# Optimization experiments

Hardware: AMD Instinct MI355X
Metric: run time of the kernel (lower is better)

Reference implementation:

```python
import jax, jax.numpy as jnp
import numpy as np

N, E, D, L, V = 200000, 500000, 128, 5, 8
BN_EPS = 1e-5


def _bn(h, g, b, m, v):
    # eval-mode BatchNorm1d with running stats
    return (h - m) * jax.lax.rsqrt(v + BN_EPS) * g + b


def setup_inputs() -> dict:
    key = jax.random.key(0)
    ks = iter(jax.random.split(key, 40))
    nk = lambda: next(ks)
    f = lambda shape: jax.random.normal(nk(), shape, jnp.float32) * 0.05
    inp = {}
    inp["x"] = jax.random.normal(nk(), (N, 12), jnp.float32)
    inp["edge_index"] = jax.random.randint(nk(), (2, E), 0, N, dtype=jnp.int32)
    inp["edge_attr"] = jax.random.randint(nk(), (E, 3), 0, V, dtype=jnp.int32)
    # atom encoder: Lin(12,D) -> BN -> ReLU -> Lin(D,D) -> BN -> ReLU -> Lin(D,D)
    inp["ae_W1"] = f((12, D)); inp["ae_b1"] = jnp.zeros((D,), jnp.float32)
    inp["ae_g1"] = jnp.ones((D,), jnp.float32); inp["ae_be1"] = jnp.zeros((D,), jnp.float32)
    inp["ae_m1"] = f((D,)); inp["ae_v1"] = jax.random.uniform(nk(), (D,), jnp.float32) + 0.5
    inp["ae_W2"] = f((D, D)); inp["ae_b2"] = jnp.zeros((D,), jnp.float32)
    inp["ae_g2"] = jnp.ones((D,), jnp.float32); inp["ae_be2"] = jnp.zeros((D,), jnp.float32)
    inp["ae_m2"] = f((D,)); inp["ae_v2"] = jax.random.uniform(nk(), (D,), jnp.float32) + 0.5
    inp["ae_W3"] = f((D, D)); inp["ae_b3"] = jnp.zeros((D,), jnp.float32)
    # per-layer GIN params (stacked over L)
    inp["bond_emb"] = f((L, 3, V, D))
    inp["eps"] = jnp.zeros((L,), jnp.float32)
    inp["mlp_W1"] = f((L, D, D)); inp["mlp_b1"] = jnp.zeros((L, D), jnp.float32)
    inp["mlp_g"] = jnp.ones((L, D), jnp.float32); inp["mlp_be"] = jnp.zeros((L, D), jnp.float32)
    inp["mlp_m"] = f((L, D)); inp["mlp_v"] = jax.random.uniform(nk(), (L, D), jnp.float32) + 0.5
    inp["mlp_W2"] = f((L, D, D)); inp["mlp_b2"] = jnp.zeros((L, D), jnp.float32)
    # per-layer outer BatchNorm
    inp["out_g"] = jnp.ones((L, D), jnp.float32); inp["out_be"] = jnp.zeros((L, D), jnp.float32)
    inp["out_m"] = f((L, D)); inp["out_v"] = jax.random.uniform(nk(), (L, D), jnp.float32) + 0.5
    return inp


def reference(x, edge_index, edge_attr,
              ae_W1, ae_b1, ae_g1, ae_be1, ae_m1, ae_v1,
              ae_W2, ae_b2, ae_g2, ae_be2, ae_m2, ae_v2,
              ae_W3, ae_b3,
              bond_emb, eps, mlp_W1, mlp_b1, mlp_g, mlp_be, mlp_m, mlp_v,
              mlp_W2, mlp_b2, out_g, out_be, out_m, out_v):
    n_nodes = x.shape[0]
    src, dst = edge_index[0], edge_index[1]
    # atom encoder
    h = jax.nn.relu(_bn(x @ ae_W1 + ae_b1, ae_g1, ae_be1, ae_m1, ae_v1))
    h = jax.nn.relu(_bn(h @ ae_W2 + ae_b2, ae_g2, ae_be2, ae_m2, ae_v2))
    h = h @ ae_W3 + ae_b3  # [N, D]
    n_layers = bond_emb.shape[0]
    for l in range(n_layers):
        # BondEncoder: sum of per-feature embeddings -> [E, D]
        be = bond_emb[l]
        e_emb = be[0][edge_attr[:, 0]] + be[1][edge_attr[:, 1]] + be[2][edge_attr[:, 2]]
        # message: relu(x_j + edge_emb); aggregate: scatter-add at dst
        msg = jax.nn.relu(h[src] + e_emb)
        agg = jax.ops.segment_sum(msg, dst, num_segments=n_nodes)
        z = (1.0 + eps[l]) * h + agg
        # GIN MLP: Lin -> BN -> ReLU -> Lin
        z = jax.nn.relu(_bn(z @ mlp_W1[l] + mlp_b1[l], mlp_g[l], mlp_be[l], mlp_m[l], mlp_v[l]))
        z = z @ mlp_W2[l] + mlp_b2[l]
        # outer BatchNorm; ReLU on all but last layer (dropout is identity in eval)
        z = _bn(z, out_g[l], out_be[l], out_m[l], out_v[l])
        if l < n_layers - 1:
            z = jax.nn.relu(z)
        h = z
    return h  # JK='last'
```

## Files before the change

kernel.cpp:

```cpp
#include <hip/hip_runtime.h>
#include <hip/hip_bf16.h>
#include <cstdint>
#include <cstddef>

#define D 128
#define NNODES 200000
#define NEDGES 500000
#define NLAYERS 5
#define BN_EPS 1e-5f
#define MAXDEG 24

typedef __attribute__((ext_vector_type(8))) short bf16x8;
typedef __attribute__((ext_vector_type(4))) float f32x4;

__device__ __forceinline__ unsigned short f2bf(float f) {
    union { float f; unsigned int u; } x; x.f = f;
    unsigned int r = (x.u + 0x7FFFu + ((x.u >> 16) & 1u)) >> 16;
    return (unsigned short)r;
}
__device__ __forceinline__ float bf2f(unsigned short u) {
    union { unsigned int u; float f; } x; x.u = ((unsigned int)u) << 16; return x.f;
}

__global__ void k_zero(int* __restrict__ p, int n) {
    int i = blockIdx.x * 256 + threadIdx.x;
    if (i < n) p[i] = 0;
}

__global__ void k_fill_edges(const int* __restrict__ ei, const int* __restrict__ ea,
                             int* __restrict__ deg, int* __restrict__ elist, int n_edges) {
    int e = blockIdx.x * 256 + threadIdx.x;
    if (e >= n_edges) return;
    int dst = ei[n_edges + e];
    int src = ei[e];
    int a0 = ea[e * 3], a1 = ea[e * 3 + 1], a2 = ea[e * 3 + 2];
    int rec = src | (a0 << 18) | (a1 << 21) | (a2 << 24);
    int pos = atomicAdd(&deg[dst], 1);
    if (pos < MAXDEG) elist[dst * MAXDEG + pos] = rec;
}

__global__ void k_prep_w(const float* __restrict__ aeW2, const float* __restrict__ aeW3,
                         const float* __restrict__ mlpW1, const float* __restrict__ mlpW2,
                         unsigned short* __restrict__ wbt) {
    int m = blockIdx.x >> 3;
    int s = (blockIdx.x & 7) * 256 + threadIdx.x;
    int f = s >> 4;
    int kc = (s & 15) * 8;
    const float* W;
    if (m == 0) W = aeW2;
    else if (m == 1) W = aeW3;
    else if (m < 7) W = mlpW1 + (size_t)(m - 2) * D * D;
    else W = mlpW2 + (size_t)(m - 7) * D * D;
    unsigned short tmp[8];
#pragma unroll
    for (int j = 0; j < 8; ++j) tmp[j] = f2bf(W[(size_t)(kc + j) * D + f]);
    *(int4*)(wbt + (size_t)m * D * D + (size_t)f * D + kc) = *(int4*)tmp;
}

__global__ void k_bondsum(const float* __restrict__ bond, unsigned short* __restrict__ bsum) {
    int idx = blockIdx.x;
    int l = idx >> 9, combo = idx & 511;
    int a0 = combo & 7, a1 = (combo >> 3) & 7, a2 = (combo >> 6) & 7;
    int f = threadIdx.x;
    const float* bl = bond + (size_t)l * 3 * 8 * 128;
    bsum[(size_t)idx * 128 + f] =
        f2bf(bl[a0 * 128 + f] + bl[1024 + a1 * 128 + f] + bl[2048 + a2 * 128 + f]);
}

__global__ void k_ae1(const float* __restrict__ x, const float* __restrict__ W,
                      const float* __restrict__ b, const float* __restrict__ g,
                      const float* __restrict__ be, const float* __restrict__ m,
                      const float* __restrict__ v, unsigned short* __restrict__ out) {
    __shared__ float sW[12][128];
    int tid = threadIdx.x;
    for (int i = tid; i < 12 * 128; i += 256) sW[i >> 7][i & 127] = W[i];
    int f0 = (tid & 31) * 4;
    int g8 = tid >> 5;
    float4 bb = *(const float4*)(b + f0);
    float4 gg = *(const float4*)(g + f0);
    float4 ee = *(const float4*)(be + f0);
    float4 mm = *(const float4*)(m + f0);
    float4 vv = *(const float4*)(v + f0);
    float A0 = gg.x * rsqrtf(vv.x + BN_EPS), S0 = (bb.x - mm.x) * A0 + ee.x;
    float A1 = gg.y * rsqrtf(vv.y + BN_EPS), S1 = (bb.y - mm.y) * A1 + ee.y;
    float A2 = gg.z * rsqrtf(vv.z + BN_EPS), S2 = (bb.z - mm.z) * A2 + ee.z;
    float A3 = gg.w * rsqrtf(vv.w + BN_EPS), S3 = (bb.w - mm.w) * A3 + ee.w;
    __syncthreads();
    for (int n = blockIdx.x * 8 + g8; n < NNODES; n += gridDim.x * 8) {
        const float4* xr = (const float4*)(x + (size_t)n * 12);
        float4 x0 = xr[0], x1 = xr[1], x2 = xr[2];
        float xv[12] = {x0.x, x0.y, x0.z, x0.w, x1.x, x1.y, x1.z, x1.w,
                        x2.x, x2.y, x2.z, x2.w};
        float a0 = 0.f, a1 = 0.f, a2 = 0.f, a3 = 0.f;
#pragma unroll
        for (int k = 0; k < 12; ++k) {
            float4 wv = *(float4*)&sW[k][f0];
            a0 += xv[k] * wv.x; a1 += xv[k] * wv.y;
            a2 += xv[k] * wv.z; a3 += xv[k] * wv.w;
        }
        unsigned short o[4];
        o[0] = f2bf(fmaxf(a0 * A0 + S0, 0.f));
        o[1] = f2bf(fmaxf(a1 * A1 + S1, 0.f));
        o[2] = f2bf(fmaxf(a2 * A2 + S2, 0.f));
        o[3] = f2bf(fmaxf(a3 * A3 + S3, 0.f));
        *(uint2*)(out + (size_t)n * D + f0) = *(uint2*)o;
    }
}

__launch_bounds__(256, 8)
__global__ void k_agg(const unsigned short* __restrict__ hin,
                      const unsigned short* __restrict__ bsum,
                      const float* __restrict__ eps_arr, int layer,
                      const int* __restrict__ deg, const int* __restrict__ elist,
                      unsigned short* __restrict__ out) {
    int tid = threadIdx.x;
    int f4 = tid & 31;
    int n = blockIdx.x * 8 + (tid >> 5);
    int dgr = min(deg[n], MAXDEG);
    int rec = (f4 < MAXDEG) ? elist[(size_t)n * MAXDEG + f4] : 0;
    float epsv = 1.f + eps_arr[layer];
    ushort4 hs = *(const ushort4*)(hin + (size_t)n * D + f4 * 4);
    float z0 = epsv * bf2f(hs.x), z1 = epsv * bf2f(hs.y);
    float z2 = epsv * bf2f(hs.z), z3 = epsv * bf2f(hs.w);

    ushort4 hv[6]; ushort4 bv[6]; int rr[6];
#pragma unroll
    for (int j = 0; j < 6; ++j) {
        rr[j] = __shfl(rec, j, 32);
        if (j < dgr) {
            hv[j] = *(const ushort4*)(hin + (size_t)(rr[j] & 0x3FFFF) * D + f4 * 4);
            bv[j] = *(const ushort4*)(bsum + (size_t)((rr[j] >> 18) & 511) * D + f4 * 4);
        }
    }
#pragma unroll
    for (int j = 0; j < 6; ++j) {
        if (j < dgr) {
            z0 += fmaxf(bf2f(hv[j].x) + bf2f(bv[j].x), 0.f);
            z1 += fmaxf(bf2f(hv[j].y) + bf2f(bv[j].y), 0.f);
            z2 += fmaxf(bf2f(hv[j].z) + bf2f(bv[j].z), 0.f);
            z3 += fmaxf(bf2f(hv[j].w) + bf2f(bv[j].w), 0.f);
        }
    }
    for (int base = 6; base < dgr; base += 4) {
        ushort4 hw[4]; ushort4 bw[4]; int rt[4];
#pragma unroll
        for (int j = 0; j < 4; ++j) {
            rt[j] = __shfl(rec, base + j, 32);
            if (base + j < dgr) {
                hw[j] = *(const ushort4*)(hin + (size_t)(rt[j] & 0x3FFFF) * D + f4 * 4);
                bw[j] = *(const ushort4*)(bsum + (size_t)((rt[j] >> 18) & 511) * D + f4 * 4);
            }
        }
#pragma unroll
        for (int j = 0; j < 4; ++j) {
            if (base + j < dgr) {
                z0 += fmaxf(bf2f(hw[j].x) + bf2f(bw[j].x), 0.f);
                z1 += fmaxf(bf2f(hw[j].y) + bf2f(bw[j].y), 0.f);
                z2 += fmaxf(bf2f(hw[j].z) + bf2f(bw[j].z), 0.f);
                z3 += fmaxf(bf2f(hw[j].w) + bf2f(bw[j].w), 0.f);
            }
        }
    }
    unsigned short o[4] = {f2bf(z0), f2bf(z1), f2bf(z2), f2bf(z3)};
    *(uint2*)(out + (size_t)n * D + f4 * 4) = *(uint2*)o;
}

#define SWZ(row, bytecol) (((row) * 256 + (bytecol)) ^ (((row) & 7) << 4))
template<int OUTF32>
__launch_bounds__(512, 6)
__global__ void k_mlp2(const unsigned short* __restrict__ hin,
                       const unsigned short* __restrict__ W1t,
                       const float* __restrict__ b1,
                       const float* __restrict__ g1, const float* __restrict__ be1,
                       const float* __restrict__ m1, const float* __restrict__ v1,
                       const unsigned short* __restrict__ W2t,
                       const float* __restrict__ b2,
                       const float* __restrict__ g2, const float* __restrict__ be2,
                       const float* __restrict__ m2, const float* __restrict__ v2,
                       unsigned short* __restrict__ outb, float* __restrict__ outf,
                       int do_bn2, int do_relu2) {
    __shared__ char sA[16384];
    __shared__ char sZ[16384];
    int tid = threadIdx.x;
    size_t nb = (size_t)blockIdx.x * 64;
    int lane = tid & 63;
    int w = tid >> 6;
    int arow = lane & 15;
    int kq = (lane >> 4) * 8;
    int c = w * 16 + arow;

    bf16x8 w1f[4], w2f[4];
#pragma unroll
    for (int kb = 0; kb < 4; ++kb) {
        w1f[kb] = *(const bf16x8*)(W1t + (size_t)c * D + kb * 32 + kq);
        w2f[kb] = *(const bf16x8*)(W2t + (size_t)c * D + kb * 32 + kq);
    }
#pragma unroll
    for (int i = 0; i < 2; ++i) {
        int s = tid + i * 512;
        int r = s >> 4, cc = (s & 15) * 16;
        *(int4*)(sA + SWZ(r, cc)) = *(const int4*)((const char*)hin + (nb + r) * 256 + cc);
    }
    __syncthreads();

    f32x4 acc[4];
#pragma unroll
    for (int rt = 0; rt < 4; ++rt) acc[rt] = (f32x4){0.f, 0.f, 0.f, 0.f};
#pragma unroll
    for (int kb = 0; kb < 4; ++kb) {
        int k0 = kb * 32 + kq;
#pragma unroll
        for (int rt = 0; rt < 4; ++rt) {
            bf16x8 a = *(bf16x8*)(sA + SWZ(rt * 16 + arow, k0 * 2));
            acc[rt] = __builtin_amdgcn_mfma_f32_16x16x32_bf16(a, w1f[kb], acc[rt], 0, 0, 0);
        }
    }

    {
        float sc = g1[c] * rsqrtf(v1[c] + BN_EPS);
        float sh = (b1[c] - m1[c]) * sc + be1[c];
#pragma unroll
        for (int rt = 0; rt < 4; ++rt) {
#pragma unroll
            for (int r = 0; r < 4; ++r) {
                int row = rt * 16 + (lane >> 4) * 4 + r;
                float z = fmaxf(acc[rt][r] * sc + sh, 0.f);
                *(unsigned short*)(sZ + SWZ(row, c * 2)) = f2bf(z);
            }
        }
    }
    __syncthreads();

#pragma unroll
    for (int rt = 0; rt < 4; ++rt) acc[rt] = (f32x4){0.f, 0.f, 0.f, 0.f};
#pragma unroll
    for (int kb = 0; kb < 4; ++kb) {
        int k0 = kb * 32 + kq;
#pragma unroll
        for (int rt = 0; rt < 4; ++rt) {
            bf16x8 a = *(bf16x8*)(sZ + SWZ(rt * 16 + arow, k0 * 2));
            acc[rt] = __builtin_amdgcn_mfma_f32_16x16x32_bf16(a, w2f[kb], acc[rt], 0, 0, 0);
        }
    }

    float sc2 = 1.f, sh2;
    if (do_bn2) { sc2 = g2[c] * rsqrtf(v2[c] + BN_EPS); sh2 = (b2[c] - m2[c]) * sc2 + be2[c]; }
    else sh2 = b2[c];
    if constexpr (OUTF32) {
#pragma unroll
        for (int rt = 0; rt < 4; ++rt) {
#pragma unroll
            for (int r = 0; r < 4; ++r) {
                int row = rt * 16 + (lane >> 4) * 4 + r;
                float z = acc[rt][r] * sc2 + sh2;
                if (do_relu2) z = fmaxf(z, 0.f);
                outf[(nb + row) * D + c] = z;
            }
        }
    } else {
#pragma unroll
        for (int rt = 0; rt < 4; ++rt) {
#pragma unroll
            for (int r = 0; r < 4; ++r) {
                int row = rt * 16 + (lane >> 4) * 4 + r;
                float z = acc[rt][r] * sc2 + sh2;
                if (do_relu2) z = fmaxf(z, 0.f);
                *(unsigned short*)(sA + SWZ(row, c * 2)) = f2bf(z);
            }
        }
        __syncthreads();
#pragma unroll
        for (int i = 0; i < 2; ++i) {
            int s = tid + i * 512;
            int r = s >> 4, cc = (s & 15) * 16;
            *(int4*)((char*)outb + (nb + r) * 256 + cc) = *(int4*)(sA + SWZ(r, cc));
        }
    }
}

extern "C" void kernel_launch(void* const* d_in, const int* in_sizes, int n_in,
                              void* d_out, int out_size, void* d_ws, size_t ws_size,
                              hipStream_t stream) {
    const float* x      = (const float*)d_in[0];
    const int*   ei     = (const int*)d_in[1];
    const int*   ea     = (const int*)d_in[2];
    const float* aeW1   = (const float*)d_in[3];
    const float* aeb1   = (const float*)d_in[4];
    const float* aeg1   = (const float*)d_in[5];
    const float* aebe1  = (const float*)d_in[6];
    const float* aem1   = (const float*)d_in[7];
    const float* aev1   = (const float*)d_in[8];
    const float* aeW2   = (const float*)d_in[9];
    const float* aeb2   = (const float*)d_in[10];
    const float* aeg2   = (const float*)d_in[11];
    const float* aebe2  = (const float*)d_in[12];
    const float* aem2   = (const float*)d_in[13];
    const float* aev2   = (const float*)d_in[14];
    const float* aeW3   = (const float*)d_in[15];
    const float* aeb3   = (const float*)d_in[16];
    const float* bond   = (const float*)d_in[17];
    const float* eps    = (const float*)d_in[18];
    const float* mlpW1  = (const float*)d_in[19];
    const float* mlpb1  = (const float*)d_in[20];
    const float* mlpg   = (const float*)d_in[21];
    const float* mlpbe  = (const float*)d_in[22];
    const float* mlpm   = (const float*)d_in[23];
    const float* mlpv   = (const float*)d_in[24];
    const float* mlpW2  = (const float*)d_in[25];
    const float* mlpb2  = (const float*)d_in[26];
    const float* outg   = (const float*)d_in[27];
    const float* outbe  = (const float*)d_in[28];
    const float* outm   = (const float*)d_in[29];
    const float* outv   = (const float*)d_in[30];

    char* ws = (char*)d_ws;
    unsigned short* hA  = (unsigned short*)ws;
    unsigned short* hB  = (unsigned short*)(ws + 51200000);
    int*   deg   = (int*)(ws + 102400000);
    int*   elist = (int*)(ws + 103200000);
    unsigned short* wbt = (unsigned short*)(ws + 122400000);
    unsigned short* bsum = (unsigned short*)(ws + 122793216);
    float* outF = (float*)d_out;

    k_zero<<<(NNODES + 255) / 256, 256, 0, stream>>>(deg, NNODES);
    k_fill_edges<<<(NEDGES + 255) / 256, 256, 0, stream>>>(ei, ea, deg, elist, NEDGES);
    k_prep_w<<<96, 256, 0, stream>>>(aeW2, aeW3, mlpW1, mlpW2, wbt);
    k_bondsum<<<NLAYERS * 512, 128, 0, stream>>>(bond, bsum);

    k_ae1<<<1280, 256, 0, stream>>>(x, aeW1, aeb1, aeg1, aebe1, aem1, aev1, hA);
    dim3 gg(NNODES / 64);
    k_mlp2<0><<<gg, 512, 0, stream>>>(hA,
        wbt + 0 * 16384, aeb2, aeg2, aebe2, aem2, aev2,
        wbt + 1 * 16384, aeb3, aeb3, aeb3, aeb3, aeb3,
        hB, nullptr, 0, 0);

    unsigned short* hc = hB;
    for (int l = 0; l < NLAYERS; ++l) {
        unsigned short* ho = (hc == hB) ? hA : hB;
        const unsigned short* W1 = wbt + (size_t)(2 + l) * 16384;
        const unsigned short* W2 = wbt + (size_t)(7 + l) * 16384;
        k_agg<<<NNODES / 8, 256, 0, stream>>>(hc, bsum + (size_t)l * 512 * 128,
                                              eps, l, deg, elist, ho);
        if (l < NLAYERS - 1) {
            k_mlp2<0><<<gg, 512, 0, stream>>>(ho,
                W1, mlpb1 + (size_t)l * D, mlpg + (size_t)l * D, mlpbe + (size_t)l * D,
                mlpm + (size_t)l * D, mlpv + (size_t)l * D,
                W2, mlpb2 + (size_t)l * D, outg + (size_t)l * D, outbe + (size_t)l * D,
                outm + (size_t)l * D, outv + (size_t)l * D,
                ho, nullptr, 1, 1);
            hc = ho;
        } else {
            k_mlp2<1><<<gg, 512, 0, stream>>>(ho,
                W1, mlpb1 + (size_t)l * D, mlpg + (size_t)l * D, mlpbe + (size_t)l * D,
                mlpm + (size_t)l * D, mlpv + (size_t)l * D,
                W2, mlpb2 + (size_t)l * D, outg + (size_t)l * D, outbe + (size_t)l * D,
                outm + (size_t)l * D, outv + (size_t)l * D,
                nullptr, outF, 1, 0);
        }
    }
    (void)in_sizes; (void)n_in; (void)out_size; (void)ws_size;
}
```

Measured before the change: 484.0 us.

## Fuse neighbor aggregation into GIN MLP kernel via shared-memory staging

Merges the per-layer aggregation kernel into the two-layer MLP kernel. Each 512-thread block now gathers neighbor messages for its 64 nodes straight into the swizzled shared tile, then runs the MFMA GEMMs. This avoids writing the aggregated features to global memory and reading them back, and saves one launch per layer. In exchange the gather runs with a lower occupancy bound and only 16 groups per block, so latency hiding for the random gathers may drop.

Result: faster. 434.6 us, median of 3 (-10.2%).

```diff
diff --git a/kernel.cpp b/kernel.cpp
--- a/kernel.cpp
+++ b/kernel.cpp
@@ -107,74 +107,15 @@
     }
 }
 
-__launch_bounds__(256, 8)
-__global__ void k_agg(const unsigned short* __restrict__ hin,
-                      const unsigned short* __restrict__ bsum,
-                      const float* __restrict__ eps_arr, int layer,
-                      const int* __restrict__ deg, const int* __restrict__ elist,
-                      unsigned short* __restrict__ out) {
-    int tid = threadIdx.x;
-    int f4 = tid & 31;
-    int n = blockIdx.x * 8 + (tid >> 5);
-    int dgr = min(deg[n], MAXDEG);
-    int rec = (f4 < MAXDEG) ? elist[(size_t)n * MAXDEG + f4] : 0;
-    float epsv = 1.f + eps_arr[layer];
-    ushort4 hs = *(const ushort4*)(hin + (size_t)n * D + f4 * 4);
-    float z0 = epsv * bf2f(hs.x), z1 = epsv * bf2f(hs.y);
-    float z2 = epsv * bf2f(hs.z), z3 = epsv * bf2f(hs.w);
-
-    ushort4 hv[6]; ushort4 bv[6]; int rr[6];
-#pragma unroll
-    for (int j = 0; j < 6; ++j) {
-        rr[j] = __shfl(rec, j, 32);
-        if (j < dgr) {
-            hv[j] = *(const ushort4*)(hin + (size_t)(rr[j] & 0x3FFFF) * D + f4 * 4);
-            bv[j] = *(const ushort4*)(bsum + (size_t)((rr[j] >> 18) & 511) * D + f4 * 4);
-        }
-    }
-#pragma unroll
-    for (int j = 0; j < 6; ++j) {
-        if (j < dgr) {
-            z0 += fmaxf(bf2f(hv[j].x) + bf2f(bv[j].x), 0.f);
-            z1 += fmaxf(bf2f(hv[j].y) + bf2f(bv[j].y), 0.f);
-            z2 += fmaxf(bf2f(hv[j].z) + bf2f(bv[j].z), 0.f);
-            z3 += fmaxf(bf2f(hv[j].w) + bf2f(bv[j].w), 0.f);
-        }
-    }
-    for (int base = 6; base < dgr; base += 4) {
-        ushort4 hw[4]; ushort4 bw[4]; int rt[4];
-#pragma unroll
-        for (int j = 0; j < 4; ++j) {
-            rt[j] = __shfl(rec, base + j, 32);
-            if (base + j < dgr) {
-                hw[j] = *(const ushort4*)(hin + (size_t)(rt[j] & 0x3FFFF) * D + f4 * 4);
-                bw[j] = *(const ushort4*)(bsum + (size_t)((rt[j] >> 18) & 511) * D + f4 * 4);
-            }
-        }
-#pragma unroll
-        for (int j = 0; j < 4; ++j) {
-            if (base + j < dgr) {
-                z0 += fmaxf(bf2f(hw[j].x) + bf2f(bw[j].x), 0.f);
-                z1 += fmaxf(bf2f(hw[j].y) + bf2f(bw[j].y), 0.f);
-                z2 += fmaxf(bf2f(hw[j].z) + bf2f(bw[j].z), 0.f);
-                z3 += fmaxf(bf2f(hw[j].w) + bf2f(bw[j].w), 0.f);
-            }
-        }
-    }
-    unsigned short o[4] = {f2bf(z0), f2bf(z1), f2bf(z2), f2bf(z3)};
-    *(uint2*)(out + (size_t)n * D + f4 * 4) = *(uint2*)o;
-}
-
 #define SWZ(row, bytecol) (((row) * 256 + (bytecol)) ^ (((row) & 7) << 4))
+
 template<int OUTF32>
 __launch_bounds__(512, 6)
 __global__ void k_mlp2(const unsigned short* __restrict__ hin,
-                       const unsigned short* __restrict__ W1t,
-                       const float* __restrict__ b1,
+                       const unsigned short* __restrict__ W1t, const float* __restrict__ b1,
                        const float* __restrict__ g1, const float* __restrict__ be1,
                        const float* __restrict__ m1, const float* __restrict__ v1,
-                       const unsigned short* __restrict__ W2t,
-                       const float* __restrict__ b2,
+                       const unsigned short* __restrict__ W2t, const float* __restrict__ b2,
                        const float* __restrict__ g2, const float* __restrict__ be2,
                        const float* __restrict__ m2, const float* __restrict__ v2,
                        unsigned short* __restrict__ outb, float* __restrict__ outf,
@@ -215,19 +156,17 @@
             acc[rt] = __builtin_amdgcn_mfma_f32_16x16x32_bf16(a, w1f[kb], acc[rt], 0, 0, 0);
         }
     }
-
     {
         float sc = g1[c] * rsqrtf(v1[c] + BN_EPS);
         float sh = (b1[c] - m1[c]) * sc + be1[c];
 #pragma unroll
-        for (int rt = 0; rt < 4; ++rt) {
+        for (int rt = 0; rt < 4; ++rt)
 #pragma unroll
             for (int r = 0; r < 4; ++r) {
                 int row = rt * 16 + (lane >> 4) * 4 + r;
                 float z = fmaxf(acc[rt][r] * sc + sh, 0.f);
                 *(unsigned short*)(sZ + SWZ(row, c * 2)) = f2bf(z);
             }
-        }
     }
     __syncthreads();
 
@@ -248,7 +187,7 @@
     else sh2 = b2[c];
     if constexpr (OUTF32) {
 #pragma unroll
-        for (int rt = 0; rt < 4; ++rt) {
+        for (int rt = 0; rt < 4; ++rt)
 #pragma unroll
             for (int r = 0; r < 4; ++r) {
                 int row = rt * 16 + (lane >> 4) * 4 + r;
@@ -256,10 +195,9 @@
                 if (do_relu2) z = fmaxf(z, 0.f);
                 outf[(nb + row) * D + c] = z;
             }
-        }
     } else {
 #pragma unroll
-        for (int rt = 0; rt < 4; ++rt) {
+        for (int rt = 0; rt < 4; ++rt)
 #pragma unroll
             for (int r = 0; r < 4; ++r) {
                 int row = rt * 16 + (lane >> 4) * 4 + r;
@@ -267,7 +205,162 @@
                 if (do_relu2) z = fmaxf(z, 0.f);
                 *(unsigned short*)(sA + SWZ(row, c * 2)) = f2bf(z);
             }
-        }
+        __syncthreads();
+#pragma unroll
+        for (int i = 0; i < 2; ++i) {
+            int s = tid + i * 512;
+            int r = s >> 4, cc = (s & 15) * 16;
+            *(int4*)((char*)outb + (nb + r) * 256 + cc) = *(int4*)(sA + SWZ(r, cc));
+        }
+    }
+}
+
+template<int OUTF32>
+__launch_bounds__(512, 5)
+__global__ void k_gin2(const unsigned short* __restrict__ hin,
+                       const unsigned short* __restrict__ bsum,
+                       const float* __restrict__ eps_arr, int layer,
+                       const int* __restrict__ deg, const int* __restrict__ elist,
+                       const unsigned short* __restrict__ W1t, const float* __restrict__ b1,
+                       const float* __restrict__ g1, const float* __restrict__ be1,
+                       const float* __restrict__ m1, const float* __restrict__ v1,
+                       const unsigned short* __restrict__ W2t, const float* __restrict__ b2,
+                       const float* __restrict__ g2, const float* __restrict__ be2,
+                       const float* __restrict__ m2, const float* __restrict__ v2,
+                       unsigned short* __restrict__ outb, float* __restrict__ outf,
+                       int do_bn2, int do_relu2) {
+    __shared__ char sA[16384];
+    __shared__ char sZ[16384];
+    int tid = threadIdx.x;
+    size_t nb = (size_t)blockIdx.x * 64;
+    int f4 = tid & 31;
+    int grp = tid >> 5;
+    float epsv = 1.f + eps_arr[layer];
+
+    for (int u = 0; u < 4; ++u) {
+        int nl = grp * 4 + u;
+        int n = (int)nb + nl;
+        int dgr = min(deg[n], MAXDEG);
+        int rec = (f4 < MAXDEG) ? elist[(size_t)n * MAXDEG + f4] : 0;
+        ushort4 hs = *(const ushort4*)(hin + (size_t)n * D + f4 * 4);
+        float z0 = epsv * bf2f(hs.x), z1 = epsv * bf2f(hs.y);
+        float z2 = epsv * bf2f(hs.z), z3 = epsv * bf2f(hs.w);
+        ushort4 hv[6]; ushort4 bv[6]; int rr[6];
+#pragma unroll
+        for (int j = 0; j < 6; ++j) {
+            rr[j] = __shfl(rec, j, 32);
+            if (j < dgr) {
+                hv[j] = *(const ushort4*)(hin + (size_t)(rr[j] & 0x3FFFF) * D + f4 * 4);
+                bv[j] = *(const ushort4*)(bsum + (size_t)((rr[j] >> 18) & 511) * D + f4 * 4);
+            }
+        }
+#pragma unroll
+        for (int j = 0; j < 6; ++j) {
+            if (j < dgr) {
+                z0 += fmaxf(bf2f(hv[j].x) + bf2f(bv[j].x), 0.f);
+                z1 += fmaxf(bf2f(hv[j].y) + bf2f(bv[j].y), 0.f);
+                z2 += fmaxf(bf2f(hv[j].z) + bf2f(bv[j].z), 0.f);
+                z3 += fmaxf(bf2f(hv[j].w) + bf2f(bv[j].w), 0.f);
+            }
+        }
+        for (int base = 6; base < dgr; base += 4) {
+            ushort4 hw[4]; ushort4 bw[4]; int rt[4];
+#pragma unroll
+            for (int j = 0; j < 4; ++j) {
+                rt[j] = __shfl(rec, base + j, 32);
+                if (base + j < dgr) {
+                    hw[j] = *(const ushort4*)(hin + (size_t)(rt[j] & 0x3FFFF) * D + f4 * 4);
+                    bw[j] = *(const ushort4*)(bsum + (size_t)((rt[j] >> 18) & 511) * D + f4 * 4);
+                }
+            }
+#pragma unroll
+            for (int j = 0; j < 4; ++j) {
+                if (base + j < dgr) {
+                    z0 += fmaxf(bf2f(hw[j].x) + bf2f(bw[j].x), 0.f);
+                    z1 += fmaxf(bf2f(hw[j].y) + bf2f(bw[j].y), 0.f);
+                    z2 += fmaxf(bf2f(hw[j].z) + bf2f(bw[j].z), 0.f);
+                    z3 += fmaxf(bf2f(hw[j].w) + bf2f(bw[j].w), 0.f);
+                }
+            }
+        }
+        unsigned short o[4] = {f2bf(z0), f2bf(z1), f2bf(z2), f2bf(z3)};
+        *(uint2*)(sA + SWZ(nl, f4 * 8)) = *(uint2*)o;
+    }
+    __syncthreads();
+
+    int lane = tid & 63;
+    int w = tid >> 6;
+    int arow = lane & 15;
+    int kq = (lane >> 4) * 8;
+    int c = w * 16 + arow;
+    bf16x8 w1f[4], w2f[4];
+#pragma unroll
+    for (int kb = 0; kb < 4; ++kb) {
+        w1f[kb] = *(const bf16x8*)(W1t + (size_t)c * D + kb * 32 + kq);
+        w2f[kb] = *(const bf16x8*)(W2t + (size_t)c * D + kb * 32 + kq);
+    }
+
+    f32x4 acc[4];
+#pragma unroll
+    for (int rt = 0; rt < 4; ++rt) acc[rt] = (f32x4){0.f, 0.f, 0.f, 0.f};
+#pragma unroll
+    for (int kb = 0; kb < 4; ++kb) {
+        int k0 = kb * 32 + kq;
+#pragma unroll
+        for (int rt = 0; rt < 4; ++rt) {
+            bf16x8 a = *(bf16x8*)(sA + SWZ(rt * 16 + arow, k0 * 2));
+            acc[rt] = __builtin_amdgcn_mfma_f32_16x16x32_bf16(a, w1f[kb], acc[rt], 0, 0, 0);
+        }
+    }
+    {
+        float sc = g1[c] * rsqrtf(v1[c] + BN_EPS);
+        float sh = (b1[c] - m1[c]) * sc + be1[c];
+#pragma unroll
+        for (int rt = 0; rt < 4; ++rt)
+#pragma unroll
+            for (int r = 0; r < 4; ++r) {
+                int row = rt * 16 + (lane >> 4) * 4 + r;
+                float z = fmaxf(acc[rt][r] * sc + sh, 0.f);
+                *(unsigned short*)(sZ + SWZ(row, c * 2)) = f2bf(z);
+            }
+    }
+    __syncthreads();
+
+#pragma unroll
+    for (int rt = 0; rt < 4; ++rt) acc[rt] = (f32x4){0.f, 0.f, 0.f, 0.f};
+#pragma unroll
+    for (int kb = 0; kb < 4; ++kb) {
+        int k0 = kb * 32 + kq;
+#pragma unroll
+        for (int rt = 0; rt < 4; ++rt) {
+            bf16x8 a = *(bf16x8*)(sZ + SWZ(rt * 16 + arow, k0 * 2));
+            acc[rt] = __builtin_amdgcn_mfma_f32_16x16x32_bf16(a, w2f[kb], acc[rt], 0, 0, 0);
+        }
+    }
+
+    float sc2 = 1.f, sh2;
+    if (do_bn2) { sc2 = g2[c] * rsqrtf(v2[c] + BN_EPS); sh2 = (b2[c] - m2[c]) * sc2 + be2[c]; }
+    else sh2 = b2[c];
+    if constexpr (OUTF32) {
+#pragma unroll
+        for (int rt = 0; rt < 4; ++rt)
+#pragma unroll
+            for (int r = 0; r < 4; ++r) {
+                int row = rt * 16 + (lane >> 4) * 4 + r;
+                float z = acc[rt][r] * sc2 + sh2;
+                if (do_relu2) z = fmaxf(z, 0.f);
+                outf[(nb + row) * D + c] = z;
+            }
+    } else {
+#pragma unroll
+        for (int rt = 0; rt < 4; ++rt)
+#pragma unroll
+            for (int r = 0; r < 4; ++r) {
+                int row = rt * 16 + (lane >> 4) * 4 + r;
+                float z = acc[rt][r] * sc2 + sh2;
+                if (do_relu2) z = fmaxf(z, 0.f);
+                *(unsigned short*)(sA + SWZ(row, c * 2)) = f2bf(z);
+            }
         __syncthreads();
 #pragma unroll
         for (int i = 0; i < 2; ++i) {
@@ -339,10 +432,9 @@
         unsigned short* ho = (hc == hB) ? hA : hB;
         const unsigned short* W1 = wbt + (size_t)(2 + l) * 16384;
         const unsigned short* W2 = wbt + (size_t)(7 + l) * 16384;
-        k_agg<<<NNODES / 8, 256, 0, stream>>>(hc, bsum + (size_t)l * 512 * 128,
-                                              eps, l, deg, elist, ho);
         if (l < NLAYERS - 1) {
-            k_mlp2<0><<<gg, 512, 0, stream>>>(ho,
+            k_gin2<0><<<gg, 512, 0, stream>>>(hc, bsum + (size_t)l * 512 * 128, eps, l,
+                deg, elist,
                 W1, mlpb1 + (size_t)l * D, mlpg + (size_t)l * D, mlpbe + (size_t)l * D,
                 mlpm + (size_t)l * D, mlpv + (size_t)l * D,
                 W2, mlpb2 + (size_t)l * D, outg + (size_t)l * D, outbe + (size_t)l * D,
@@ -350,7 +442,8 @@
                 ho, nullptr, 1, 1);
             hc = ho;
         } else {
-            k_mlp2<1><<<gg, 512, 0, stream>>>(ho,
+            k_gin2<1><<<gg, 512, 0, stream>>>(hc, bsum + (size_t)l * 512 * 128, eps, l,
+                deg, elist,
                 W1, mlpb1 + (size_t)l * D, mlpg + (size_t)l * D, mlpbe + (size_t)l * D,
                 mlpm + (size_t)l * D, mlpv + (size_t)l * D,
                 W2, mlpb2 + (size_t)l * D, outg + (size_t)l * D, outbe + (size_t)l * D,
```
